# Optimization experiments

Hardware: AMD Instinct MI355X
Metric: run time of the kernel (lower is better)

The kernel has to match this reference:

```python
import jax, jax.numpy as jnp
import numpy as np

EPS = 1e-5

def _ln(x, g, b):
    mu = jnp.mean(x, axis=-1, keepdims=True)
    var = jnp.mean(jnp.square(x - mu), axis=-1, keepdims=True)
    return (x - mu) * jax.lax.rsqrt(var + EPS) * g + b

def _mha(xq, xkv, Wq, bq, Wk, bk, Wv, bv, Wo, bo, causal):
    # Wq/Wk/Wv: [H,E,D]; per-head linear projections (no 1/sqrt(d) scaling, faithful to source)
    q = jnp.einsum('bse,hed->bhsd', xq, Wq) + bq[None, :, None, :]
    k = jnp.einsum('bte,hed->bhtd', xkv, Wk) + bk[None, :, None, :]
    v = jnp.einsum('bte,hed->bhtd', xkv, Wv) + bv[None, :, None, :]
    s = jnp.einsum('bhsd,bhtd->bhst', q, k)
    if causal:
        S, T = s.shape[-2], s.shape[-1]
        keep = jnp.tril(jnp.ones((S, T), dtype=bool))  # intended causal mask (source had inverted-mask bug -> NaNs)
        s = jnp.where(keep[None, None], s, jnp.finfo(s.dtype).min)
    w = jax.nn.softmax(s, axis=-1)
    o = jnp.einsum('bhst,bhtd->bhsd', w, v)
    B, H, S, D = o.shape
    o = o.transpose(0, 2, 1, 3).reshape(B, S, H * D)  # concat heads in order, matches torch.cat
    return o @ Wo + bo

def setup_inputs() -> dict:
    B, S, T, E, H, D, F = 4, 1024, 1024, 1024, 16, 64, 4096
    key = jax.random.key(0)
    ks = iter(jax.random.split(key, 40))
    def w(shape, scale=0.02):
        return (scale * jax.random.normal(next(ks), shape)).astype(jnp.float32)
    inp = {
        'x': w((B, S, E), 1.0),
        'enc': w((B, T, E), 1.0),
        'ln1_g': jnp.ones((E,), jnp.float32), 'ln1_b': jnp.zeros((E,), jnp.float32),
        'ln2_g': jnp.ones((E,), jnp.float32), 'ln2_b': jnp.zeros((E,), jnp.float32),
        'ln3_g': jnp.ones((E,), jnp.float32), 'ln3_b': jnp.zeros((E,), jnp.float32),
        'Wq1': w((H, E, D)), 'bq1': jnp.zeros((H, D), jnp.float32),
        'Wk1': w((H, E, D)), 'bk1': jnp.zeros((H, D), jnp.float32),
        'Wv1': w((H, E, D)), 'bv1': jnp.zeros((H, D), jnp.float32),
        'Wo1': w((E, E)), 'bo1': jnp.zeros((E,), jnp.float32),
        'Wq2': w((H, E, D)), 'bq2': jnp.zeros((H, D), jnp.float32),
        'Wk2': w((H, E, D)), 'bk2': jnp.zeros((H, D), jnp.float32),
        'Wv2': w((H, E, D)), 'bv2': jnp.zeros((H, D), jnp.float32),
        'Wo2': w((E, E)), 'bo2': jnp.zeros((E,), jnp.float32),
        'Wup': w((E, F)), 'bup': jnp.zeros((F,), jnp.float32),
        'Wdown': w((F, E)), 'bdown': jnp.zeros((E,), jnp.float32),
    }
    return inp

def reference(x, enc, ln1_g, ln1_b, ln2_g, ln2_b, ln3_g, ln3_b,
              Wq1, bq1, Wk1, bk1, Wv1, bv1, Wo1, bo1,
              Wq2, bq2, Wk2, bk2, Wv2, bv2, Wo2, bo2,
              Wup, bup, Wdown, bdown):
    h = _ln(x, ln1_g, ln1_b)
    x = x + _mha(h, h, Wq1, bq1, Wk1, bk1, Wv1, bv1, Wo1, bo1, causal=True)
    h = _ln(x, ln2_g, ln2_b)
    x = x + _mha(h, enc, Wq2, bq2, Wk2, bk2, Wv2, bv2, Wo2, bo2, causal=False)
    h = _ln(x, ln3_g, ln3_b)
    ff = jax.nn.gelu(h @ Wup + bup, approximate=False) @ Wdown + bdown  # dropout is identity in eval
    return x + ff
```

## Files before the change

### kernel.cpp

```cpp
#include <hip/hip_runtime.h>
#include <math.h>

typedef unsigned short u16;
typedef __bf16  bf16x8 __attribute__((ext_vector_type(8)));
typedef float   f32x4  __attribute__((ext_vector_type(4)));

__device__ __forceinline__ u16 f2bf(float f) {
  unsigned u = __float_as_uint(f);
  u += 0x7fffu + ((u >> 16) & 1u);
  return (u16)(u >> 16);
}
__device__ __forceinline__ __bf16 f2bfv(float f) {
  return __builtin_bit_cast(__bf16, f2bf(f));
}
__device__ __forceinline__ void gl_lds16(const void* g, void* l) {
  __builtin_amdgcn_global_load_lds((__attribute__((address_space(1))) void*)(void*)g,
                                   (__attribute__((address_space(3))) void*)l, 16u, 0, 0u);
}
__device__ __forceinline__ f32x4 mfma16(bf16x8 a, bf16x8 b, f32x4 c) {
  return __builtin_amdgcn_mfma_f32_16x16x32_bf16(a, b, c, 0, 0, 0);
}

__global__ __launch_bounds__(256) void ln_kernel(const float* __restrict__ x,
    const float* __restrict__ g, const float* __restrict__ b, u16* __restrict__ out) {
  const long row = blockIdx.x;
  const int t = threadIdx.x;
  const float4 v = ((const float4*)(x + row * 1024))[t];
  float s  = v.x + v.y + v.z + v.w;
  float sq = v.x*v.x + v.y*v.y + v.z*v.z + v.w*v.w;
#pragma unroll
  for (int m = 1; m < 64; m <<= 1) { s += __shfl_xor(s, m); sq += __shfl_xor(sq, m); }
  __shared__ float ss[4], ssq[4];
  const int wave = t >> 6;
  if ((t & 63) == 0) { ss[wave] = s; ssq[wave] = sq; }
  __syncthreads();
  s  = ss[0] + ss[1] + ss[2] + ss[3];
  sq = ssq[0] + ssq[1] + ssq[2] + ssq[3];
  const float mu = s * (1.0f / 1024.0f);
  const float rs = rsqrtf(sq * (1.0f / 1024.0f) - mu * mu + 1e-5f);
  const float4 gg = ((const float4*)g)[t];
  const float4 bb = ((const float4*)b)[t];
  ushort4 o;
  o.x = f2bf((v.x - mu) * rs * gg.x + bb.x);
  o.y = f2bf((v.y - mu) * rs * gg.y + bb.y);
  o.z = f2bf((v.z - mu) * rs * gg.z + bb.z);
  o.w = f2bf((v.w - mu) * rs * gg.w + bb.w);
  ((ushort4*)(out + row * 1024))[t] = o;
}

__global__ __launch_bounds__(256) void cast_kernel(const float* __restrict__ in, u16* __restrict__ out) {
  const long i = ((long)blockIdx.x * 256 + threadIdx.x) * 4;
  const float4 v = *(const float4*)(in + i);
  ushort4 o;
  o.x = f2bf(v.x); o.y = f2bf(v.y); o.z = f2bf(v.z); o.w = f2bf(v.w);
  *(ushort4*)(out + i) = o;
}

__global__ __launch_bounds__(256) void tp_kernel(const float* __restrict__ in,
    u16* __restrict__ out, int C, long in_bs, long out_bs, int out_ld) {
  __shared__ u16 tile[64][65];
  in  += (long)blockIdx.z * in_bs;
  out += (long)blockIdx.z * out_bs;
  const int r0 = blockIdx.y << 6, c0 = blockIdx.x << 6;
  const int t = threadIdx.x;
  const int lr = t >> 4, lc = (t & 15) << 2;
#pragma unroll
  for (int i = 0; i < 4; i++) {
    const int row = lr + i * 16;
    const float4 v = *(const float4*)(in + (long)(r0 + row) * C + c0 + lc);
    tile[row][lc + 0] = f2bf(v.x); tile[row][lc + 1] = f2bf(v.y);
    tile[row][lc + 2] = f2bf(v.z); tile[row][lc + 3] = f2bf(v.w);
  }
  __syncthreads();
#pragma unroll
  for (int i = 0; i < 4; i++) {
    const int cc = lr + i * 16;
    ushort4 o;
    o.x = tile[lc + 0][cc]; o.y = tile[lc + 1][cc];
    o.z = tile[lc + 2][cc]; o.w = tile[lc + 3][cc];
    *(ushort4*)(out + (long)(c0 + cc) * out_ld + r0 + lc) = o;
  }
}

template<int MFRAG, int MODE>
__global__ __launch_bounds__(256, 2) void gemm_kernel(
    const u16* __restrict__ A, const u16* __restrict__ BT,
    const float* __restrict__ b0, const float* __restrict__ b1, const float* __restrict__ b2,
    const float* __restrict__ res,
    u16* __restrict__ o0, u16* __restrict__ o1, u16* __restrict__ o2,
    float* __restrict__ of, int M, int N, int K)
{
  constexpr int BM = MFRAG * 32;
  __shared__ __bf16 As[BM * 64];
  __shared__ __bf16 Bs[128 * 64];
  const int tid = threadIdx.x;
  const int wave = tid >> 6, lane = tid & 63;
  const int g = lane >> 4, li = lane & 15;
  const long m0 = (long)blockIdx.y * BM;
  const int  n0 = blockIdx.x << 7;
  const int  wr = wave >> 1, wc = wave & 1;

  f32x4 acc[MFRAG][4] = {};

  const u16* Ag = A + (m0 + wave * (MFRAG * 8) + (lane >> 3)) * K + ((lane & 7) << 3);
  const u16* Bg = BT + ((long)(n0 + wave * 32 + (lane >> 3))) * K + ((lane & 7) << 3);
  __bf16* AsW = As + wave * (MFRAG * 512);
  __bf16* BsW = Bs + wave * 2048;

  for (int k0 = 0; k0 < K; k0 += 64) {
#pragma unroll
    for (int i = 0; i < MFRAG; i++)
      gl_lds16(Ag + (long)i * 8 * K + k0, AsW + i * 512);
#pragma unroll
    for (int i = 0; i < 4; i++)
      gl_lds16(Bg + (long)i * 8 * K + k0, BsW + i * 512);
    __syncthreads();
#pragma unroll
    for (int kk = 0; kk < 2; kk++) {
      bf16x8 af[MFRAG], bv[4];
#pragma unroll
      for (int m = 0; m < MFRAG; m++)
        af[m] = *(const bf16x8*)&As[(wr * (MFRAG * 16) + m * 16 + li) * 64 + kk * 32 + g * 8];
#pragma unroll
      for (int n = 0; n < 4; n++)
        bv[n] = *(const bf16x8*)&Bs[(wc * 64 + n * 16 + li) * 64 + kk * 32 + g * 8];
#pragma unroll
      for (int m = 0; m < MFRAG; m++)
#pragma unroll
        for (int n = 0; n < 4; n++)
          acc[m][n] = mfma16(af[m], bv[n], acc[m][n]);
    }
    __syncthreads();
  }

#pragma unroll
  for (int m = 0; m < MFRAG; m++) {
#pragma unroll
    for (int n = 0; n < 4; n++) {
      const int col = n0 + wc * 64 + n * 16 + li;
#pragma unroll
      for (int r = 0; r < 4; r++) {
        const int row = (int)m0 + wr * (MFRAG * 16) + m * 16 + g * 4 + r;
        float v = acc[m][n][r];
        if constexpr (MODE == 0) {
          const int sel = col >> 10, cl = col & 1023;
          v += (sel == 0 ? b0 : sel == 1 ? b1 : b2)[cl];
          const int bI = row >> 10, sI = row & 1023, hI = cl >> 6, dI = cl & 63;
          if (sel < 2) (sel == 0 ? o0 : o1)[((long)(bI * 16 + hI) * 1024 + sI) * 64 + dI] = f2bf(v);
          else         o2[((long)(bI * 16 + hI) * 64 + dI) * 1024 + sI] = f2bf(v);
        } else if constexpr (MODE == 1) {
          const int sel = col >> 10, cl = col & 1023;
          v += (sel == 0 ? b0 : b1)[cl];
          const int bI = row >> 10, sI = row & 1023, hI = cl >> 6, dI = cl & 63;
          if (sel == 0) o0[((long)(bI * 16 + hI) * 1024 + sI) * 64 + dI] = f2bf(v);
          else          o1[((long)(bI * 16 + hI) * 64 + dI) * 1024 + sI] = f2bf(v);
        } else if constexpr (MODE == 2) {
          v += b0[col];
          const int bI = row >> 10, sI = row & 1023, hI = col >> 6, dI = col & 63;
          o0[((long)(bI * 16 + hI) * 1024 + sI) * 64 + dI] = f2bf(v);
        } else if constexpr (MODE == 3) {
          v += b0[col];
          const long idx = (long)row * N + col;
          of[idx] = v + res[idx];
        } else {
          v += b0[col];
          const float gl = 0.5f * v * (1.0f + erff(v * 0.70710678118654752f));
          o0[(long)row * N + col] = f2bf(gl);
        }
      }
    }
  }
}

__global__ __launch_bounds__(256, 2) void attn_kernel(
    const u16* __restrict__ Q, const u16* __restrict__ Kb,
    const u16* __restrict__ VT, u16* __restrict__ O, const int causal)
{
  __shared__ __bf16 Ks[32 * 64];
  __shared__ __bf16 Vs[64 * 32];
  __shared__ __bf16 Ps[4][512];
  const int tid = threadIdx.x;
  const int wave = tid >> 6, lane = tid & 63;
  const int g = lane >> 4, li = lane & 15;
  const int qt = blockIdx.x, bh = blockIdx.y;
  const int b_ = bh >> 4, h_ = bh & 15;
  const int q_lo = qt * 64 + wave * 16;

  const u16* Qp = Q + ((long)bh * 1024 + q_lo + li) * 64 + g * 8;
  const bf16x8 aq0 = *(const bf16x8*)Qp;
  const bf16x8 aq1 = *(const bf16x8*)(Qp + 32);

  f32x4 acc[4] = {};
  float mrun[4] = {-1e30f, -1e30f, -1e30f, -1e30f};
  float lrun[4] = {0.f, 0.f, 0.f, 0.f};

  const u16* Kg = Kb + ((long)bh * 1024 + wave * 8 + (lane >> 3)) * 64 + ((lane & 7) << 3);
  const u16* Vg = VT + ((long)bh * 64 + wave * 16 + (lane >> 2)) * 1024 + ((lane & 3) << 3);
  __bf16* KsW = Ks + wave * 512;
  __bf16* VsW = Vs + wave * 512;

  const int nk = causal ? (qt + 1) * 2 : 32;
  for (int kt = 0; kt < nk; kt++) {
    const int k0 = kt * 32;
    gl_lds16(Kg + (long)k0 * 64, KsW);
    gl_lds16(Vg + k0, VsW);
    __syncthreads();

    f32x4 s0 = {}, s1 = {};
    {
      const bf16x8 b00 = *(const bf16x8*)&Ks[(li) * 64 + g * 8];
      const bf16x8 b01 = *(const bf16x8*)&Ks[(li) * 64 + 32 + g * 8];
      const bf16x8 b10 = *(const bf16x8*)&Ks[(16 + li) * 64 + g * 8];
      const bf16x8 b11 = *(const bf16x8*)&Ks[(16 + li) * 64 + 32 + g * 8];
      s0 = mfma16(aq0, b00, s0); s0 = mfma16(aq1, b01, s0);
      s1 = mfma16(aq0, b10, s1); s1 = mfma16(aq1, b11, s1);
    }
    if (causal && (k0 + 31 > q_lo)) {
#pragma unroll
      for (int r = 0; r < 4; r++) {
        const int q = q_lo + g * 4 + r;
        if (k0 + li > q)      s0[r] = -1e30f;
        if (k0 + 16 + li > q) s1[r] = -1e30f;
      }
    }
#pragma unroll
    for (int r = 0; r < 4; r++) {
      float pm = fmaxf(s0[r], s1[r]);
      pm = fmaxf(pm, __shfl_xor(pm, 1));
      pm = fmaxf(pm, __shfl_xor(pm, 2));
      pm = fmaxf(pm, __shfl_xor(pm, 4));
      pm = fmaxf(pm, __shfl_xor(pm, 8));
      const float mnew = fmaxf(mrun[r], pm);
      const float p0 = expf(s0[r] - mnew);
      const float p1 = expf(s1[r] - mnew);
      Ps[wave][(g * 4 + r) * 32 + li]      = f2bfv(p0);
      Ps[wave][(g * 4 + r) * 32 + 16 + li] = f2bfv(p1);
      float rsum = p0 + p1;
      rsum += __shfl_xor(rsum, 1);
      rsum += __shfl_xor(rsum, 2);
      rsum += __shfl_xor(rsum, 4);
      rsum += __shfl_xor(rsum, 8);
      const float sc = expf(mrun[r] - mnew);
      mrun[r] = mnew;
      lrun[r] = lrun[r] * sc + rsum;
      acc[0][r] *= sc; acc[1][r] *= sc; acc[2][r] *= sc; acc[3][r] *= sc;
    }
    const bf16x8 pa = *(const bf16x8*)&Ps[wave][li * 32 + g * 8];
#pragma unroll
    for (int n = 0; n < 4; n++) {
      const bf16x8 bv = *(const bf16x8*)&Vs[(n * 16 + li) * 32 + g * 8];
      acc[n] = mfma16(pa, bv, acc[n]);
    }
    __syncthreads();
  }

#pragma unroll
  for (int r = 0; r < 4; r++) {
    const int q = q_lo + g * 4 + r;
    const float inv = 1.0f / lrun[r];
#pragma unroll
    for (int n = 0; n < 4; n++)
      O[((long)b_ * 1024 + q) * 1024 + h_ * 64 + n * 16 + li] = f2bf(acc[n][r] * inv);
  }
}

extern "C" void kernel_launch(void* const* d_in, const int* in_sizes, int n_in,
                              void* d_out, int out_size, void* d_ws, size_t ws_size,
                              hipStream_t stream) {
  const float* x     = (const float*)d_in[0];
  const float* enc   = (const float*)d_in[1];
  const float* ln1_g = (const float*)d_in[2];
  const float* ln1_b = (const float*)d_in[3];
  const float* ln2_g = (const float*)d_in[4];
  const float* ln2_b = (const float*)d_in[5];
  const float* ln3_g = (const float*)d_in[6];
  const float* ln3_b = (const float*)d_in[7];
  const float* Wq1 = (const float*)d_in[8];  const float* bq1 = (const float*)d_in[9];
  const float* Wk1 = (const float*)d_in[10]; const float* bk1 = (const float*)d_in[11];
  const float* Wv1 = (const float*)d_in[12]; const float* bv1 = (const float*)d_in[13];
  const float* Wo1 = (const float*)d_in[14]; const float* bo1 = (const float*)d_in[15];
  const float* Wq2 = (const float*)d_in[16]; const float* bq2 = (const float*)d_in[17];
  const float* Wk2 = (const float*)d_in[18]; const float* bk2 = (const float*)d_in[19];
  const float* Wv2 = (const float*)d_in[20]; const float* bv2 = (const float*)d_in[21];
  const float* Wo2 = (const float*)d_in[22]; const float* bo2 = (const float*)d_in[23];
  const float* Wup = (const float*)d_in[24]; const float* bup = (const float*)d_in[25];
  const float* Wdn = (const float*)d_in[26]; const float* bdn = (const float*)d_in[27];

  char* ws = (char*)d_ws;
  const size_t MB = 1ull << 20;
  u16*   wpack  = (u16*)(ws);
  u16*   enc_bf = (u16*)(ws + 8 * MB);
  u16*   h_bf   = (u16*)(ws + 16 * MB);
  u16*   Qb     = (u16*)(ws + 24 * MB);
  u16*   Kbf    = (u16*)(ws + 32 * MB);
  u16*   VTb    = (u16*)(ws + 40 * MB);
  u16*   att_o  = (u16*)(ws + 48 * MB);
  float* x2     = (float*)(ws + 56 * MB);
  float* x3     = (float*)(ws + 72 * MB);
  u16*   ffmid  = (u16*)(ws + 24 * MB);

  const dim3 T(256);

  ln_kernel<<<4096, T, 0, stream>>>(x, ln1_g, ln1_b, h_bf);
  cast_kernel<<<4096, T, 0, stream>>>(enc, enc_bf);
  tp_kernel<<<dim3(1, 16, 16), T, 0, stream>>>(Wq1, wpack,              64, 65536L, 65536L, 1024);
  tp_kernel<<<dim3(1, 16, 16), T, 0, stream>>>(Wk1, wpack + 1024 * 1024, 64, 65536L, 65536L, 1024);
  tp_kernel<<<dim3(1, 16, 16), T, 0, stream>>>(Wv1, wpack + 2048 * 1024, 64, 65536L, 65536L, 1024);
  gemm_kernel<4, 0><<<dim3(24, 32), T, 0, stream>>>(h_bf, wpack, bq1, bk1, bv1, nullptr,
      Qb, Kbf, VTb, nullptr, 4096, 3072, 1024);
  attn_kernel<<<dim3(16, 64), T, 0, stream>>>(Qb, Kbf, VTb, att_o, 1);
  tp_kernel<<<dim3(16, 16, 1), T, 0, stream>>>(Wo1, wpack, 1024, 0L, 0L, 1024);
  gemm_kernel<2, 3><<<dim3(8, 64), T, 0, stream>>>(att_o, wpack, bo1, nullptr, nullptr, x,
      nullptr, nullptr, nullptr, x2, 4096, 1024, 1024);

  ln_kernel<<<4096, T, 0, stream>>>(x2, ln2_g, ln2_b, h_bf);
  tp_kernel<<<dim3(1, 16, 16), T, 0, stream>>>(Wq2, wpack, 64, 65536L, 65536L, 1024);
  gemm_kernel<2, 2><<<dim3(8, 64), T, 0, stream>>>(h_bf, wpack, bq2, nullptr, nullptr, nullptr,
      Qb, nullptr, nullptr, nullptr, 4096, 1024, 1024);
  tp_kernel<<<dim3(1, 16, 16), T, 0, stream>>>(Wk2, wpack,              64, 65536L, 65536L, 1024);
  tp_kernel<<<dim3(1, 16, 16), T, 0, stream>>>(Wv2, wpack + 1024 * 1024, 64, 65536L, 65536L, 1024);
  gemm_kernel<4, 1><<<dim3(16, 32), T, 0, stream>>>(enc_bf, wpack, bk2, bv2, nullptr, nullptr,
      Kbf, VTb, nullptr, nullptr, 4096, 2048, 1024);
  attn_kernel<<<dim3(16, 64), T, 0, stream>>>(Qb, Kbf, VTb, att_o, 0);
  tp_kernel<<<dim3(16, 16, 1), T, 0, stream>>>(Wo2, wpack, 1024, 0L, 0L, 1024);
  gemm_kernel<2, 3><<<dim3(8, 64), T, 0, stream>>>(att_o, wpack, bo2, nullptr, nullptr, x2,
      nullptr, nullptr, nullptr, x3, 4096, 1024, 1024);

  ln_kernel<<<4096, T, 0, stream>>>(x3, ln3_g, ln3_b, h_bf);
  tp_kernel<<<dim3(64, 16, 1), T, 0, stream>>>(Wup, wpack, 4096, 0L, 0L, 1024);
  gemm_kernel<4, 4><<<dim3(32, 32), T, 0, stream>>>(h_bf, wpack, bup, nullptr, nullptr, nullptr,
      ffmid, nullptr, nullptr, nullptr, 4096, 4096, 1024);
  tp_kernel<<<dim3(16, 64, 1), T, 0, stream>>>(Wdn, wpack, 1024, 0L, 0L, 4096);
  gemm_kernel<2, 3><<<dim3(8, 64), T, 0, stream>>>(ffmid, wpack, bdn, nullptr, nullptr, x3,
      nullptr, nullptr, nullptr, (float*)d_out, 4096, 1024, 4096);
}
```

Before: 699.3 us.

## Double-buffer attention K/V tiles with 64-key blocks, swizzled LDS, lazy rescale

The attention kernel now processes 64 keys per iteration instead of 32 and double-buffers K and V tiles in LDS, prefetching the next tile while computing on the current one. This removes one barrier-bound load per step. The QKV GEMM epilogue writes K and V^T with an XOR swizzle so that LDS reads are bank-conflict free. Softmax rescaling is skipped unless the running max grows by more than a threshold, and it uses fast __expf. This adds LDS use (about 40KB per block), which may lower occupancy, and the lazy rescale slightly changes numerics.

```diff
diff --git a/kernel.cpp b/kernel.cpp
--- a/kernel.cpp
+++ b/kernel.cpp
@@ -9,9 +9,6 @@
   unsigned u = __float_as_uint(f);
   u += 0x7fffu + ((u >> 16) & 1u);
   return (u16)(u >> 16);
-}
-__device__ __forceinline__ __bf16 f2bfv(float f) {
-  return __builtin_bit_cast(__bf16, f2bf(f));
 }
 __device__ __forceinline__ void gl_lds16(const void* g, void* l) {
   __builtin_amdgcn_global_load_lds((__attribute__((address_space(1))) void*)(void*)g,
@@ -142,18 +139,22 @@
       for (int r = 0; r < 4; r++) {
         const int row = (int)m0 + wr * (MFRAG * 16) + m * 16 + g * 4 + r;
         float v = acc[m][n][r];
-        if constexpr (MODE == 0) {
+        if constexpr (MODE == 0 || MODE == 1) {
           const int sel = col >> 10, cl = col & 1023;
-          v += (sel == 0 ? b0 : sel == 1 ? b1 : b2)[cl];
+          v += (MODE == 0 ? (sel == 0 ? b0 : sel == 1 ? b1 : b2)
+                          : (sel == 0 ? b0 : b1))[cl];
           const int bI = row >> 10, sI = row & 1023, hI = cl >> 6, dI = cl & 63;
-          if (sel < 2) (sel == 0 ? o0 : o1)[((long)(bI * 16 + hI) * 1024 + sI) * 64 + dI] = f2bf(v);
-          else         o2[((long)(bI * 16 + hI) * 64 + dI) * 1024 + sI] = f2bf(v);
-        } else if constexpr (MODE == 1) {
-          const int sel = col >> 10, cl = col & 1023;
-          v += (sel == 0 ? b0 : b1)[cl];
-          const int bI = row >> 10, sI = row & 1023, hI = cl >> 6, dI = cl & 63;
-          if (sel == 0) o0[((long)(bI * 16 + hI) * 1024 + sI) * 64 + dI] = f2bf(v);
-          else          o1[((long)(bI * 16 + hI) * 64 + dI) * 1024 + sI] = f2bf(v);
+          const long bhI = (long)(bI * 16 + hI);
+          const int qsel = (MODE == 0) ? 0 : -1;
+          if (sel == qsel) {
+            o0[(bhI * 1024 + sI) * 64 + dI] = f2bf(v);
+          } else if (sel == qsel + 1) {
+            u16* Kp = (MODE == 0) ? o1 : o0;
+            Kp[(bhI * 1024 + sI) * 64 + (dI ^ ((sI & 7) << 3))] = f2bf(v);
+          } else {
+            u16* Vp = (MODE == 0) ? o2 : o1;
+            Vp[(bhI * 64 + dI) * 1024 + (sI & ~63) + ((sI & 63) ^ ((dI & 7) << 3))] = f2bf(v);
+          }
         } else if constexpr (MODE == 2) {
           v += b0[col];
           const int bI = row >> 10, sI = row & 1023, hI = col >> 6, dI = col & 63;
@@ -176,9 +177,9 @@
     const u16* __restrict__ Q, const u16* __restrict__ Kb,
     const u16* __restrict__ VT, u16* __restrict__ O, const int causal)
 {
-  __shared__ __bf16 Ks[32 * 64];
-  __shared__ __bf16 Vs[64 * 32];
-  __shared__ __bf16 Ps[4][512];
+  __shared__ u16 Ks[2][4096];
+  __shared__ u16 Vs[2][4096];
+  __shared__ u16 Ps[4][1024];
   const int tid = threadIdx.x;
   const int wave = tid >> 6, lane = tid & 63;
   const int g = lane >> 4, li = lane & 15;
@@ -194,62 +195,107 @@
   float mrun[4] = {-1e30f, -1e30f, -1e30f, -1e30f};
   float lrun[4] = {0.f, 0.f, 0.f, 0.f};
 
-  const u16* Kg = Kb + ((long)bh * 1024 + wave * 8 + (lane >> 3)) * 64 + ((lane & 7) << 3);
-  const u16* Vg = VT + ((long)bh * 64 + wave * 16 + (lane >> 2)) * 1024 + ((lane & 3) << 3);
-  __bf16* KsW = Ks + wave * 512;
-  __bf16* VsW = Vs + wave * 512;
-
-  const int nk = causal ? (qt + 1) * 2 : 32;
+  const u16* Kbh = Kb + (long)bh * 65536;
+  const u16* Vbh = VT + (long)bh * 65536;
+  const int swl = (li & 7) << 3;
+
+  const int nk = causal ? (qt + 1) : 16;
+
+#pragma unroll
+  for (int i = 0; i < 2; i++) {
+    const int bc = i * 256 + wave * 64;
+    gl_lds16(Kbh + (long)(bc + lane) * 8, &Ks[0][bc * 8]);
+    const int ci = bc + lane, d = ci >> 3, c = ci & 7;
+    gl_lds16(Vbh + (long)d * 1024 + c * 8, &Vs[0][bc * 8]);
+  }
+  __syncthreads();
+
   for (int kt = 0; kt < nk; kt++) {
-    const int k0 = kt * 32;
-    gl_lds16(Kg + (long)k0 * 64, KsW);
-    gl_lds16(Vg + k0, VsW);
-    __syncthreads();
-
-    f32x4 s0 = {}, s1 = {};
-    {
-      const bf16x8 b00 = *(const bf16x8*)&Ks[(li) * 64 + g * 8];
-      const bf16x8 b01 = *(const bf16x8*)&Ks[(li) * 64 + 32 + g * 8];
-      const bf16x8 b10 = *(const bf16x8*)&Ks[(16 + li) * 64 + g * 8];
-      const bf16x8 b11 = *(const bf16x8*)&Ks[(16 + li) * 64 + 32 + g * 8];
-      s0 = mfma16(aq0, b00, s0); s0 = mfma16(aq1, b01, s0);
-      s1 = mfma16(aq0, b10, s1); s1 = mfma16(aq1, b11, s1);
-    }
-    if (causal && (k0 + 31 > q_lo)) {
-#pragma unroll
-      for (int r = 0; r < 4; r++) {
-        const int q = q_lo + g * 4 + r;
-        if (k0 + li > q)      s0[r] = -1e30f;
-        if (k0 + 16 + li > q) s1[r] = -1e30f;
+    const int buf = kt & 1;
+    const int k0 = kt * 64;
+    if (kt + 1 < nk) {
+      const int nb = buf ^ 1;
+#pragma unroll
+      for (int i = 0; i < 2; i++) {
+        const int bc = i * 256 + wave * 64;
+        gl_lds16(Kbh + (long)(kt + 1) * 4096 + (long)(bc + lane) * 8, &Ks[nb][bc * 8]);
+        const int ci = bc + lane, d = ci >> 3, c = ci & 7;
+        gl_lds16(Vbh + (long)d * 1024 + (kt + 1) * 64 + c * 8, &Vs[nb][bc * 8]);
       }
     }
+
+    f32x4 s[4] = {};
+#pragma unroll
+    for (int n = 0; n < 4; n++) {
+      const u16* kp = &Ks[buf][(n * 16 + li) * 64];
+      const bf16x8 bk0 = *(const bf16x8*)(kp + ((g * 8) ^ swl));
+      const bf16x8 bk1 = *(const bf16x8*)(kp + ((32 + g * 8) ^ swl));
+      s[n] = mfma16(aq0, bk0, s[n]);
+      s[n] = mfma16(aq1, bk1, s[n]);
+    }
+
+    if (causal && k0 + 63 > q_lo) {
+#pragma unroll
+      for (int n = 0; n < 4; n++) {
+        const int key = k0 + n * 16 + li;
+#pragma unroll
+        for (int r = 0; r < 4; r++)
+          if (key > q_lo + g * 4 + r) s[n][r] = -1e30f;
+      }
+    }
+
+    float pmax[4];
 #pragma unroll
     for (int r = 0; r < 4; r++) {
-      float pm = fmaxf(s0[r], s1[r]);
+      float pm = fmaxf(fmaxf(s[0][r], s[1][r]), fmaxf(s[2][r], s[3][r]));
       pm = fmaxf(pm, __shfl_xor(pm, 1));
       pm = fmaxf(pm, __shfl_xor(pm, 2));
       pm = fmaxf(pm, __shfl_xor(pm, 4));
       pm = fmaxf(pm, __shfl_xor(pm, 8));
-      const float mnew = fmaxf(mrun[r], pm);
-      const float p0 = expf(s0[r] - mnew);
-      const float p1 = expf(s1[r] - mnew);
-      Ps[wave][(g * 4 + r) * 32 + li]      = f2bfv(p0);
-      Ps[wave][(g * 4 + r) * 32 + 16 + li] = f2bfv(p1);
-      float rsum = p0 + p1;
-      rsum += __shfl_xor(rsum, 1);
-      rsum += __shfl_xor(rsum, 2);
-      rsum += __shfl_xor(rsum, 4);
-      rsum += __shfl_xor(rsum, 8);
-      const float sc = expf(mrun[r] - mnew);
-      mrun[r] = mnew;
-      lrun[r] = lrun[r] * sc + rsum;
-      acc[0][r] *= sc; acc[1][r] *= sc; acc[2][r] *= sc; acc[3][r] *= sc;
-    }
-    const bf16x8 pa = *(const bf16x8*)&Ps[wave][li * 32 + g * 8];
+      pmax[r] = pm;
+    }
+    const bool need = (pmax[0] > mrun[0] + 8.f) || (pmax[1] > mrun[1] + 8.f) ||
+                      (pmax[2] > mrun[2] + 8.f) || (pmax[3] > mrun[3] + 8.f);
+    if (__any(need)) {
+#pragma unroll
+      for (int r = 0; r < 4; r++) {
+        const float mnew = fmaxf(mrun[r], pmax[r]);
+        const float sc = __expf(mrun[r] - mnew);
+        mrun[r] = mnew;
+        lrun[r] *= sc;
+        acc[0][r] *= sc; acc[1][r] *= sc; acc[2][r] *= sc; acc[3][r] *= sc;
+      }
+    }
+#pragma unroll
+    for (int r = 0; r < 4; r++) {
+      const int q = g * 4 + r;
+      const int swq = (q & 7) << 3;
+      const float p0 = __expf(s[0][r] - mrun[r]);
+      const float p1 = __expf(s[1][r] - mrun[r]);
+      const float p2 = __expf(s[2][r] - mrun[r]);
+      const float p3 = __expf(s[3][r] - mrun[r]);
+      u16* pw = &Ps[wave][q * 64];
+      pw[(li)      ^ swq] = f2bf(p0);
+      pw[(16 + li) ^ swq] = f2bf(p1);
+      pw[(32 + li) ^ swq] = f2bf(p2);
+      pw[(48 + li) ^ swq] = f2bf(p3);
+      float rs_ = (p0 + p1) + (p2 + p3);
+      rs_ += __shfl_xor(rs_, 1);
+      rs_ += __shfl_xor(rs_, 2);
+      rs_ += __shfl_xor(rs_, 4);
+      rs_ += __shfl_xor(rs_, 8);
+      lrun[r] += rs_;
+    }
+
+    const bf16x8 pa0 = *(const bf16x8*)&Ps[wave][li * 64 + ((g * 8) ^ swl)];
+    const bf16x8 pa1 = *(const bf16x8*)&Ps[wave][li * 64 + ((32 + g * 8) ^ swl)];
 #pragma unroll
     for (int n = 0; n < 4; n++) {
-      const bf16x8 bv = *(const bf16x8*)&Vs[(n * 16 + li) * 32 + g * 8];
-      acc[n] = mfma16(pa, bv, acc[n]);
+      const u16* vp = &Vs[buf][(n * 16 + li) * 64];
+      const bf16x8 v0 = *(const bf16x8*)(vp + ((g * 8) ^ swl));
+      const bf16x8 v1 = *(const bf16x8*)(vp + ((32 + g * 8) ^ swl));
+      acc[n] = mfma16(pa0, v0, acc[n]);
+      acc[n] = mfma16(pa1, v1, acc[n]);
     }
     __syncthreads();
   }
@@ -303,7 +349,7 @@
 
   ln_kernel<<<4096, T, 0, stream>>>(x, ln1_g, ln1_b, h_bf);
   cast_kernel<<<4096, T, 0, stream>>>(enc, enc_bf);
-  tp_kernel<<<dim3(1, 16, 16), T, 0, stream>>>(Wq1, wpack,              64, 65536L, 65536L, 1024);
+  tp_kernel<<<dim3(1, 16, 16), T, 0, stream>>>(Wq1, wpack,               64, 65536L, 65536L, 1024);
   tp_kernel<<<dim3(1, 16, 16), T, 0, stream>>>(Wk1, wpack + 1024 * 1024, 64, 65536L, 65536L, 1024);
   tp_kernel<<<dim3(1, 16, 16), T, 0, stream>>>(Wv1, wpack + 2048 * 1024, 64, 65536L, 65536L, 1024);
   gemm_kernel<4, 0><<<dim3(24, 32), T, 0, stream>>>(h_bf, wpack, bq1, bk1, bv1, nullptr,
@@ -317,7 +363,7 @@
   tp_kernel<<<dim3(1, 16, 16), T, 0, stream>>>(Wq2, wpack, 64, 65536L, 65536L, 1024);
   gemm_kernel<2, 2><<<dim3(8, 64), T, 0, stream>>>(h_bf, wpack, bq2, nullptr, nullptr, nullptr,
       Qb, nullptr, nullptr, nullptr, 4096, 1024, 1024);
-  tp_kernel<<<dim3(1, 16, 16), T, 0, stream>>>(Wk2, wpack,              64, 65536L, 65536L, 1024);
+  tp_kernel<<<dim3(1, 16, 16), T, 0, stream>>>(Wk2, wpack,               64, 65536L, 65536L, 1024);
   tp_kernel<<<dim3(1, 16, 16), T, 0, stream>>>(Wv2, wpack + 1024 * 1024, 64, 65536L, 65536L, 1024);
   gemm_kernel<4, 1><<<dim3(16, 32), T, 0, stream>>>(enc_bf, wpack, bk2, bv2, nullptr, nullptr,
       Kbf, VTb, nullptr, nullptr, 4096, 2048, 1024);
```

After: 604.1 us. -13.6%, faster.
